# Kernel optimization log

Measured on AMD Instinct MI355X. Metric: run time of the kernel, lower is better.

## Reference

```python
import jax, jax.numpy as jnp
import numpy as np


def setup_inputs() -> dict:
    B, S, DK, DV, H = 2, 2048, 1024, 1024, 16
    ks = jax.random.split(jax.random.key(0), 7)
    keys = jax.random.normal(ks[0], (B, S, DK), jnp.float32)
    queries = jax.random.normal(ks[1], (B, S, DK), jnp.float32)
    values = jax.random.normal(ks[2], (B, S, DV), jnp.float32)
    # per-head projection weights, stored as [H, in, out] (torch Linear uses W.T; math-equivalent)
    WQ = jax.random.normal(ks[3], (H, DK, DK // H), jnp.float32) / np.sqrt(DK).astype(np.float32)
    WK = jax.random.normal(ks[4], (H, DK, DK // H), jnp.float32) / np.sqrt(DK).astype(np.float32)
    WV = jax.random.normal(ks[5], (H, DV, DV // H), jnp.float32) / np.sqrt(DV).astype(np.float32)
    WO = jax.random.normal(ks[6], (DV, DV), jnp.float32) / np.sqrt(DV).astype(np.float32)
    return {"keys": keys, "queries": queries, "values": values,
            "WQ": WQ, "WK": WK, "WV": WV, "WO": WO, "masking": 1}


def reference(keys, queries, values, WQ, WK, WV, WO, masking):
    B, Sq, _ = queries.shape
    Sk = keys.shape[1]
    # batched per-head projections (original loops over heads in Python)
    Q = jnp.einsum('bqd,hde->bhqe', queries, WQ)   # [B,H,Sq,dh]
    K = jnp.einsum('bkd,hde->bhke', keys, WK)      # [B,H,Sk,dh]
    V = jnp.einsum('bkd,hde->bhke', values, WV)    # [B,H,Sk,dvh]
    q_idx = jnp.arange(Sq)[:, None]
    k_idx = jnp.arange(Sk)[None, :]
    causal = k_idx <= q_idx
    # NOTE: original never applies the slope m; bias = (i - j) for i<=j else 0, same for all heads
    bias = jnp.where(causal, (k_idx - q_idx).astype(jnp.float32), 0.0)
    scale = np.float32(1.0 / np.sqrt(Sk))  # original divides by sqrt(keys.shape[1])
    y = (jnp.einsum('bhqe,bhke->bhqk', Q, K) + bias) * scale
    if masking:
        y = jnp.where(causal, y, -jnp.inf)
    # original: F.softmax(y, 1) on [B,Sq,Sk] -> softmax over the QUERY axis
    z = jax.nn.softmax(y, axis=2)
    out = jnp.einsum('bhqk,bhke->bhqe', z, V)      # [B,H,Sq,dvh]
    out = out.transpose(0, 2, 1, 3).reshape(B, Sq, -1)  # concat heads on last dim
    return out @ WO
```

## Files before the change

### kernel.cpp

```cpp
#include <hip/hip_runtime.h>
#include <math.h>

#define SEQ    2048
#define DMODEL 1024
#define NH     16
#define DH     64
#define NB     2
#define BHN    (NB*NH)

static constexpr float SCALE = 0.02209708691207961f;

typedef __attribute__((ext_vector_type(8))) short short8;
typedef __attribute__((ext_vector_type(4))) short short4v;
typedef __attribute__((ext_vector_type(4))) float f32x4;

__device__ __forceinline__ short f2bf(float f) {
    union { float f; unsigned u; } v; v.f = f;
    unsigned r = (v.u + 0x7FFFu + ((v.u >> 16) & 1u)) >> 16;
    return (short)r;
}

__device__ __forceinline__ unsigned pack_bf2(float a, float b) {
    union { float f; unsigned u; } ua, ub; ua.f = a; ub.f = b;
    return __builtin_amdgcn_perm(ub.u + 0x8000u, ua.u + 0x8000u, 0x07060302u);
}

__device__ __forceinline__ float bf2f(short s) {
    union { unsigned u; float f; } v; v.u = ((unsigned)(unsigned short)s) << 16;
    return v.f;
}

__device__ __forceinline__ void load16_lds(const short* g, short* l) {
    __builtin_amdgcn_global_load_lds(
        (const __attribute__((address_space(1))) unsigned int*)g,
        (__attribute__((address_space(3))) unsigned int*)l,
        16, 0, 0);
}

__device__ __forceinline__ void stage_rows(const short* g, short* s, int t, int ldg, int nIter) {
    int wave = t >> 6, lane = t & 63;
    #pragma unroll
    for (int i = 0; i < 4; ++i) {
        if (i >= nIter) break;
        int E   = i * 2048 + wave * 512 + lane * 8;
        int row = E >> 6;
        int blk = (lane & 7) ^ (row & 7);
        load16_lds(g + (size_t)row * ldg + blk * 8, s + i * 2048 + wave * 512);
    }
}

__device__ __forceinline__ short8 frag_sw(const short* s, int rowbase, int ks, int lane) {
    int m   = rowbase + (lane & 15);
    int q   = lane >> 4;
    int blk = (ks * 4 + q) ^ (m & 7);
    return *(const short8*)(s + m * 64 + blk * 8);
}

__global__ __launch_bounds__(256) void convert_x(
    const float* __restrict__ q, const float* __restrict__ k, const float* __restrict__ v,
    short* __restrict__ Xq, short* __restrict__ Xk, short* __restrict__ Xv)
{
    const int z = blockIdx.z;
    const float* src = (z == 0) ? q : (z == 1) ? k : v;
    short* dst = (z == 0) ? Xq : (z == 1) ? Xk : Xv;
    size_t idx = ((size_t)blockIdx.x * 256 + threadIdx.x) * 8;
    float4 a = *(const float4*)(src + idx);
    float4 b = *(const float4*)(src + idx + 4);
    short8 o;
    o[0] = f2bf(a.x); o[1] = f2bf(a.y); o[2] = f2bf(a.z); o[3] = f2bf(a.w);
    o[4] = f2bf(b.x); o[5] = f2bf(b.y); o[6] = f2bf(b.z); o[7] = f2bf(b.w);
    *(short8*)(dst + idx) = o;
}

__global__ __launch_bounds__(256) void convert_w(
    const float* __restrict__ WQ, const float* __restrict__ WK,
    const float* __restrict__ WV, const float* __restrict__ WO,
    short* __restrict__ WQt, short* __restrict__ WKt,
    short* __restrict__ WVt, short* __restrict__ WOt)
{
    const int z = blockIdx.z;
    const int k0 = blockIdx.x * 64;
    const int ny = blockIdx.y;
    const float* W = (z == 0) ? WQ : (z == 1) ? WK : (z == 2) ? WV : WO;
    short* Wt = (z == 0) ? WQt : (z == 1) ? WKt : (z == 2) ? WVt : WOt;

    __shared__ float Ts[64][68];
    const int t = threadIdx.x;
    const int tr = t >> 4, tc4 = (t & 15) * 4;

    #pragma unroll
    for (int i = 0; i < 4; ++i) {
        int row = tr + i * 16;
        float4 v;
        if (z < 3) v = *(const float4*)(W + (size_t)ny * DMODEL * DH + (size_t)(k0 + row) * DH + tc4);
        else       v = *(const float4*)(W + (size_t)(k0 + row) * DMODEL + ny * 64 + tc4);
        Ts[tc4 + 0][row] = v.x; Ts[tc4 + 1][row] = v.y;
        Ts[tc4 + 2][row] = v.z; Ts[tc4 + 3][row] = v.w;
    }
    __syncthreads();
    #pragma unroll
    for (int i = 0; i < 4; ++i) {
        int nl = tr + i * 16;
        short4v o;
        o[0] = f2bf(Ts[nl][tc4 + 0]); o[1] = f2bf(Ts[nl][tc4 + 1]);
        o[2] = f2bf(Ts[nl][tc4 + 2]); o[3] = f2bf(Ts[nl][tc4 + 3]);
        *(short4v*)(Wt + (size_t)(ny * 64 + nl) * DMODEL + k0 + tc4) = o;
    }
}

__global__ __launch_bounds__(256) void gemm_nt(
    const short* __restrict__ A0, const short* __restrict__ A1, const short* __restrict__ A2,
    const short* __restrict__ B0, const short* __restrict__ B1, const short* __restrict__ B2,
    short* __restrict__ Y0, short* __restrict__ Y1, short* __restrict__ Y2,
    float* __restrict__ outF, float* __restrict__ outF2, int phase)
{
    const int z = blockIdx.z;
    const short* X  = (phase == 1) ? A0 : (z == 0) ? A0 : (z == 1) ? A1 : A2;
    const short* Wt = (phase == 1) ? B0 : (z == 0) ? B0 : (z == 1) ? B1 : B2;
    short* Y        = (z == 0) ? Y0 : (z == 1) ? Y1 : Y2;
    const bool vOrient = (phase == 0) && (z == 2);

    const int lin = blockIdx.y * 8 + blockIdx.x;
    const int n0 = (lin >> 5) * 128;
    const int m0 = (lin & 31) * 128;

    __shared__ short As[128 * 64];
    __shared__ short Bs[128 * 64];

    const int t = threadIdx.x;
    const int wave = t >> 6, lane = t & 63;
    const int wrow = (wave >> 1) * 64, wcol = (wave & 1) * 64;
    const int quad = lane >> 4, l15 = lane & 15;

    f32x4 acc[4][4];
    #pragma unroll
    for (int i = 0; i < 4; ++i)
        #pragma unroll
        for (int j = 0; j < 4; ++j)
            acc[i][j] = (f32x4)0.f;

    const int kBeg = (phase == 1) ? (z * 512) : 0;
    const int kEnd = (phase == 1) ? (z * 512 + 512) : DMODEL;
    for (int k0 = kBeg; k0 < kEnd; k0 += 64) {
        __syncthreads();
        stage_rows(X  + (size_t)m0 * DMODEL + k0, As, t, DMODEL, 4);
        stage_rows(Wt + (size_t)n0 * DMODEL + k0, Bs, t, DMODEL, 4);
        __syncthreads();
        if (!vOrient) {
            #pragma unroll
            for (int ks = 0; ks < 2; ++ks) {
                short8 xf[4], wf[4];
                #pragma unroll
                for (int i = 0; i < 4; ++i) xf[i] = frag_sw(As, wrow + i * 16, ks, lane);
                #pragma unroll
                for (int i = 0; i < 4; ++i) wf[i] = frag_sw(Bs, wcol + i * 16, ks, lane);
                #pragma unroll
                for (int a = 0; a < 4; ++a)
                    #pragma unroll
                    for (int b = 0; b < 4; ++b)
                        acc[a][b] = __builtin_amdgcn_mfma_f32_16x16x32_bf16(
                            wf[a], xf[b], acc[a][b], 0, 0, 0);
            }
        } else {
            #pragma unroll
            for (int ks = 0; ks < 2; ++ks) {
                short8 xf[4], wf[4];
                #pragma unroll
                for (int i = 0; i < 4; ++i) xf[i] = frag_sw(As, wrow + i * 16, ks, lane);
                #pragma unroll
                for (int i = 0; i < 4; ++i) wf[i] = frag_sw(Bs, wcol + i * 16, ks, lane);
                #pragma unroll
                for (int a = 0; a < 4; ++a)
                    #pragma unroll
                    for (int b = 0; b < 4; ++b)
                        acc[a][b] = __builtin_amdgcn_mfma_f32_16x16x32_bf16(
                            xf[a], wf[b], acc[a][b], 0, 0, 0);
            }
        }
    }

    if (vOrient) {
        #pragma unroll
        for (int a = 0; a < 4; ++a) {
            #pragma unroll
            for (int b = 0; b < 4; ++b) {
                int m = m0 + wrow + a * 16 + quad * 4;
                int n = n0 + wcol + b * 16 + l15;
                int bb = m >> 11, s = m & 2047, h = n >> 6, e = n & 63;
                short4v o;
                #pragma unroll
                for (int i = 0; i < 4; ++i) o[i] = f2bf(acc[a][b][i]);
                *(short4v*)(Y + ((size_t)((bb * NH + h) * DH + e)) * SEQ + s) = o;
            }
        }
    } else if (phase == 1) {
        float* dst = (z == 0) ? outF : outF2;
        #pragma unroll
        for (int a = 0; a < 4; ++a) {
            #pragma unroll
            for (int b = 0; b < 4; ++b) {
                int n = n0 + wcol + a * 16 + quad * 4;
                int m = m0 + wrow + b * 16 + l15;
                float4 o = make_float4(acc[a][b][0], acc[a][b][1], acc[a][b][2], acc[a][b][3]);
                *(float4*)(dst + (size_t)m * DMODEL + n) = o;
            }
        }
    } else {
        #pragma unroll
        for (int a = 0; a < 4; ++a) {
            #pragma unroll
            for (int b = 0; b < 4; ++b) {
                int n = n0 + wcol + a * 16 + quad * 4;
                int m = m0 + wrow + b * 16 + l15;
                int bb = m >> 11, s = m & 2047, h = n >> 6, e = n & 63;
                short4v o;
                #pragma unroll
                for (int i = 0; i < 4; ++i) o[i] = f2bf(acc[a][b][i]);
                *(short4v*)(Y + ((size_t)((bb * NH + h) * SEQ + s)) * DH + e) = o;
            }
        }
    }
}

__global__ __launch_bounds__(256) void reduce_add(
    float* __restrict__ dst, const float* __restrict__ src)
{
    size_t i = ((size_t)blockIdx.x * 256 + threadIdx.x) * 8;
    float4 a0 = *(float4*)(dst + i);
    float4 a1 = *(float4*)(dst + i + 4);
    float4 b0 = *(const float4*)(src + i);
    float4 b1 = *(const float4*)(src + i + 4);
    a0.x += b0.x; a0.y += b0.y; a0.z += b0.z; a0.w += b0.w;
    a1.x += b1.x; a1.y += b1.y; a1.z += b1.z; a1.w += b1.w;
    *(float4*)(dst + i) = a0;
    *(float4*)(dst + i + 4) = a1;
}

__global__ __launch_bounds__(256) void stats_mfma(
    const short* __restrict__ Qg, const short* __restrict__ Kg,
    float* __restrict__ rDg, const int* __restrict__ mask_p)
{
    const int gblk = blockIdx.x;
    const int masking = mask_p[0];

    __shared__ short Ks[64 * 64];
    __shared__ short Qs[2][128 * 64];

    const int t = threadIdx.x;
    const int wave = t >> 6, lane = t & 63;
    const int quad = lane >> 4, l15 = lane & 15;

    for (int item = 0; item < 2; ++item) {
        const int w  = item ? (1023 - gblk) : gblk;
        const int kt = w >> 5, bh = w & 31;
        const int k0 = kt * 64;

        const int qb0 = masking ? (kt >> 1) : 0;
        const int q0s = qb0 * 128;
        if (item) __syncthreads();
        stage_rows(Kg + ((size_t)bh * SEQ + k0) * DH, Ks, t, DH, 2);
        stage_rows(Qg + ((size_t)bh * SEQ + q0s) * DH, Qs[0], t, DH, 4);
        __syncthreads();

        short8 Kf[2];
        Kf[0] = frag_sw(Ks, wave * 16, 0, lane);
        Kf[1] = frag_sw(Ks, wave * 16, 1, lane);

        int   kgi[4];
        float biasK[4];
        #pragma unroll
        for (int i = 0; i < 4; ++i) {
            kgi[i] = k0 + wave * 16 + quad * 4 + i;
            biasK[i] = SCALE * (float)kgi[i];
        }
        float qS[8];
        #pragma unroll
        for (int nt = 0; nt < 8; ++nt)
            qS[nt] = SCALE * (float)(q0s + nt * 16 + l15);

        float dsum[4] = {0.f, 0.f, 0.f, 0.f};
        const int nIter = masking ? (16 - qb0) : 16;
        for (int it = 0; it < nIter; ++it) {
            const int cur = it & 1;
            if (it > 0) __syncthreads();
            if (it + 1 < nIter)
                stage_rows(Qg + ((size_t)bh * SEQ + q0s + (it + 1) * 128) * DH, Qs[1 - cur], t, DH, 4);

            f32x4 acc[8];
            #pragma unroll
            for (int nt = 0; nt < 8; ++nt) acc[nt] = (f32x4)0.f;
            __builtin_amdgcn_s_setprio(1);
            #pragma unroll
            for (int ks = 0; ks < 2; ++ks)
                #pragma unroll
                for (int nt = 0; nt < 8; ++nt)
                    acc[nt] = __builtin_amdgcn_mfma_f32_16x16x32_bf16(
                        Kf[ks], frag_sw(Qs[cur], nt * 16, ks, lane), acc[nt], 0, 0, 0);
            __builtin_amdgcn_s_setprio(0);

            const bool exact = masking && (it == 0);
            #pragma unroll
            for (int nt = 0; nt < 8; ++nt) {
                #pragma unroll
                for (int i = 0; i < 4; ++i) {
                    float diff = biasK[i] - qS[nt];
                    float v = masking ? fmaf(acc[nt][i], SCALE, diff)
                                      : fmaf(acc[nt][i], SCALE, fminf(diff, 0.f));
                    float e = __expf(v);
                    if (exact)
                        e = (kgi[i] <= (q0s + nt * 16 + l15)) ? e : 0.f;
                    dsum[i] += e;
                }
            }
            #pragma unroll
            for (int nt = 0; nt < 8; ++nt) qS[nt] += 128.f * SCALE;
        }

        #pragma unroll
        for (int i = 0; i < 4; ++i) {
            float d = dsum[i];
            #pragma unroll
            for (int mm = 1; mm < 16; mm <<= 1) d += __shfl_xor(d, mm);
            dsum[i] = d;
        }
        if (l15 == 0) {
            const int kc = k0 + wave * 16 + quad * 4;
            float4 o = make_float4(1.f / dsum[0], 1.f / dsum[1], 1.f / dsum[2], 1.f / dsum[3]);
            *(float4*)(rDg + (size_t)bh * SEQ + kc) = o;
        }
    }
}

__global__ __launch_bounds__(256) void scale_vt(
    short* __restrict__ Vt, const float* __restrict__ rDg)
{
    size_t base = ((size_t)blockIdx.x * 256 + threadIdx.x) * 8;
    int s = (int)(base & (SEQ - 1));
    int bh = (int)(base >> 17);
    short8 v = *(short8*)(Vt + base);
    const float* rp = rDg + (size_t)bh * SEQ + s;
    float4 r0 = *(const float4*)rp;
    float4 r1 = *(const float4*)(rp + 4);
    float rr[8] = {r0.x, r0.y, r0.z, r0.w, r1.x, r1.y, r1.z, r1.w};
    union { unsigned u[4]; short8 s8; } o;
    #pragma unroll
    for (int j = 0; j < 4; ++j)
        o.u[j] = pack_bf2(bf2f(v[2 * j]) * rr[2 * j], bf2f(v[2 * j + 1]) * rr[2 * j + 1]);
    *(short8*)(Vt + base) = o.s8;
}

template<int MODE>
__device__ __forceinline__ void attn_tile(
    const short* Kbuf, const short* Vbuf, short* Pw,
    const short8 Qf[2], const float bias[4][4], f32x4 oacc[4],
    int lane, int quad, int l15, int qloc)
{
    f32x4 sacc[4];
    #pragma unroll
    for (int mt = 0; mt < 4; ++mt) sacc[mt] = (f32x4)0.f;
    __builtin_amdgcn_s_setprio(1);
    #pragma unroll
    for (int ks = 0; ks < 2; ++ks) {
        #pragma unroll
        for (int mt = 0; mt < 4; ++mt)
            sacc[mt] = __builtin_amdgcn_mfma_f32_16x16x32_bf16(
                frag_sw(Kbuf, mt * 16, ks, lane), Qf[ks], sacc[mt], 0, 0, 0);
    }
    __builtin_amdgcn_s_setprio(0);
    __asm__ volatile("" ::: "memory");
    #pragma unroll
    for (int mt = 0; mt < 4; ++mt) {
        float p[4];
        #pragma unroll
        for (int i = 0; i < 4; ++i) {
            float bi = bias[mt][i];
            float v = (MODE == 2) ? fmaf(sacc[mt][i], SCALE, fminf(bi, 0.f))
                                  : fmaf(sacc[mt][i], SCALE, bi);
            float e = __expf(v);
            if (MODE == 1)
                e = ((mt * 16 + quad * 4 + i) <= qloc) ? e : 0.f;
            p[i] = e;
        }
        int blk = (2 * mt + (quad >> 1)) ^ (l15 & 7);
        *(uint2*)(Pw + l15 * 64 + blk * 8 + (quad & 1) * 4) =
            make_uint2(pack_bf2(p[0], p[1]), pack_bf2(p[2], p[3]));
    }
    __asm__ volatile("" ::: "memory");
    __builtin_amdgcn_s_setprio(1);
    #pragma unroll
    for (int ks = 0; ks < 2; ++ks) {
        short8 pf = *(const short8*)(Pw + l15 * 64 + (((ks * 4 + quad) ^ (l15 & 7)) * 8));
        #pragma unroll
        for (int mt = 0; mt < 4; ++mt)
            oacc[mt] = __builtin_amdgcn_mfma_f32_16x16x32_bf16(
                frag_sw(Vbuf, mt * 16, ks, lane), pf, oacc[mt], 0, 0, 0);
    }
    __builtin_amdgcn_s_setprio(0);
}

__global__ __launch_bounds__(256) void attn_mfma(
    const short* __restrict__ Qg, const short* __restrict__ Kg, const short* __restrict__ Vt,
    short* __restrict__ attnb, const int* __restrict__ mask_p)
{
    const int gblk = blockIdx.x;
    const int masking = mask_p[0];

    __shared__ short Qs[64 * 64];
    __shared__ short Ks[2][64 * 64];
    __shared__ short Vts[2][64 * 64];

    const int t = threadIdx.x;
    const int wave = t >> 6, lane = t & 63;
    const int quad = lane >> 4, l15 = lane & 15;
    short* Pw = Qs + wave * 1024;
    const int qloc = wave * 16 + l15;

    for (int item = 0; item < 2; ++item) {
        const int w  = item ? (1023 - gblk) : gblk;
        const int qt = w >> 5, bh = w & 31;
        const int b = bh >> 4, h = bh & (NH - 1);
        const int q0 = qt * 64;

        if (item) __syncthreads();
        stage_rows(Qg + ((size_t)bh * SEQ + q0) * DH, Qs, t, DH, 2);
        stage_rows(Kg + (size_t)bh * SEQ * DH, Ks[0], t, DH, 2);
        stage_rows(Vt + (size_t)bh * DH * SEQ, Vts[0], t, SEQ, 2);
        __syncthreads();

        short8 Qf[2];
        Qf[0] = frag_sw(Qs, wave * 16, 0, lane);
        Qf[1] = frag_sw(Qs, wave * 16, 1, lane);

        float bias[4][4];
        #pragma unroll
        for (int mt = 0; mt < 4; ++mt)
            #pragma unroll
            for (int i = 0; i < 4; ++i)
                bias[mt][i] = SCALE * (float)((mt * 16 + quad * 4 + i)
                                            - (q0 + qloc));

        f32x4 oacc[4];
        #pragma unroll
        for (int mt = 0; mt < 4; ++mt) oacc[mt] = (f32x4)0.f;

        const int nIter = masking ? (qt + 1) : (SEQ / 64);
        for (int it = 0; it < nIter; ++it) {
            const int cur = it & 1;
            if (it > 0) __syncthreads();
            if (it + 1 < nIter) {
                const int k0n = (it + 1) * 64;
                stage_rows(Kg + ((size_t)bh * SEQ + k0n) * DH, Ks[1 - cur], t, DH, 2);
                stage_rows(Vt + (size_t)bh * DH * SEQ + k0n, Vts[1 - cur], t, SEQ, 2);
            }
            if (!masking)       attn_tile<2>(Ks[cur], Vts[cur], Pw, Qf, bias, oacc, lane, quad, l15, qloc);
            else if (it == qt)  attn_tile<1>(Ks[cur], Vts[cur], Pw, Qf, bias, oacc, lane, quad, l15, qloc);
            else                attn_tile<0>(Ks[cur], Vts[cur], Pw, Qf, bias, oacc, lane, quad, l15, qloc);
            #pragma unroll
            for (int mt = 0; mt < 4; ++mt)
                #pragma unroll
                for (int i = 0; i < 4; ++i)
                    bias[mt][i] += 64.f * SCALE;
        }

        #pragma unroll
        for (int mt = 0; mt < 4; ++mt) {
            int e = mt * 16 + quad * 4;
            int q = q0 + wave * 16 + l15;
            short4v o;
            #pragma unroll
            for (int i = 0; i < 4; ++i) o[i] = f2bf(oacc[mt][i]);
            *(short4v*)(attnb + ((size_t)(b * SEQ + q)) * DMODEL + h * DH + e) = o;
        }
    }
}

extern "C" void kernel_launch(void* const* d_in, const int* in_sizes, int n_in,
                              void* d_out, int out_size, void* d_ws, size_t ws_size,
                              hipStream_t stream) {
    const float* keys    = (const float*)d_in[0];
    const float* queries = (const float*)d_in[1];
    const float* values  = (const float*)d_in[2];
    const float* WQ      = (const float*)d_in[3];
    const float* WK      = (const float*)d_in[4];
    const float* WV      = (const float*)d_in[5];
    const float* WO      = (const float*)d_in[6];
    const int*   mask_p  = (const int*)d_in[7];
    float* out = (float*)d_out;

    const size_t nX = (size_t)NB * SEQ * DMODEL;
    const size_t nW = (size_t)DMODEL * DMODEL;
    const size_t nQ = (size_t)BHN * SEQ * DH;

    short* ws = (short*)d_ws;
    short* Xq    = ws;
    short* Xk    = Xq + nX;
    short* Xv    = Xk + nX;
    short* WQt   = Xv + nX;
    short* WKt   = WQt + nW;
    short* WVt   = WKt + nW;
    short* WOt   = WVt + nW;
    short* Qg    = WOt + nW;
    short* Kg    = Qg + nQ;
    short* Vtg   = Kg + nQ;
    short* attnb = Vtg + nQ;
    float* rDg   = (float*)(attnb + nX);
    float* outP1 = (float*)ws;

    convert_x<<<dim3(2048, 1, 3), dim3(256), 0, stream>>>(queries, keys, values, Xq, Xk, Xv);
    convert_w<<<dim3(16, 16, 4), dim3(256), 0, stream>>>(WQ, WK, WV, WO, WQt, WKt, WVt, WOt);
    gemm_nt<<<dim3(8, 32, 3), dim3(256), 0, stream>>>(
        Xq, Xk, Xv, WQt, WKt, WVt, Qg, Kg, Vtg, nullptr, nullptr, 0);
    stats_mfma<<<dim3(512), dim3(256), 0, stream>>>(Qg, Kg, rDg, mask_p);
    scale_vt<<<dim3(2048), dim3(256), 0, stream>>>(Vtg, rDg);
    attn_mfma<<<dim3(512), dim3(256), 0, stream>>>(Qg, Kg, Vtg, attnb, mask_p);
    gemm_nt<<<dim3(8, 32, 2), dim3(256), 0, stream>>>(
        attnb, nullptr, nullptr, WOt, nullptr, nullptr, nullptr, nullptr, nullptr, out, outP1, 1);
    reduce_add<<<dim3(2048), dim3(256), 0, stream>>>(out, outP1);
}
```

Measured before the change: 258.0 us.

## Fold column-normalizer into attention P and double-buffer output projection GEMM

Drops the separate scale_vt kernel. The per-key reciprocal denominators are instead applied to the exponentiated scores inside attn_tile, which saves a full read-modify-write pass over V and one launch. The output projection gets its own kernel, gemm_out, with double-buffered shared-memory staging so loads overlap the MFMA work; the phase branches leave gemm_nt. In exchange the attention inner loop does an extra global float4 load per tile, and gemm_out doubles its LDS use, which may lower occupancy.

```diff
diff --git a/kernel.cpp b/kernel.cpp
--- a/kernel.cpp
+++ b/kernel.cpp
@@ -111,14 +111,13 @@
 __global__ __launch_bounds__(256) void gemm_nt(
     const short* __restrict__ A0, const short* __restrict__ A1, const short* __restrict__ A2,
     const short* __restrict__ B0, const short* __restrict__ B1, const short* __restrict__ B2,
-    short* __restrict__ Y0, short* __restrict__ Y1, short* __restrict__ Y2,
-    float* __restrict__ outF, float* __restrict__ outF2, int phase)
+    short* __restrict__ Y0, short* __restrict__ Y1, short* __restrict__ Y2)
 {
     const int z = blockIdx.z;
-    const short* X  = (phase == 1) ? A0 : (z == 0) ? A0 : (z == 1) ? A1 : A2;
-    const short* Wt = (phase == 1) ? B0 : (z == 0) ? B0 : (z == 1) ? B1 : B2;
+    const short* X  = (z == 0) ? A0 : (z == 1) ? A1 : A2;
+    const short* Wt = (z == 0) ? B0 : (z == 1) ? B1 : B2;
     short* Y        = (z == 0) ? Y0 : (z == 1) ? Y1 : Y2;
-    const bool vOrient = (phase == 0) && (z == 2);
+    const bool vOrient = (z == 2);
 
     const int lin = blockIdx.y * 8 + blockIdx.x;
     const int n0 = (lin >> 5) * 128;
@@ -139,9 +138,7 @@
         for (int j = 0; j < 4; ++j)
             acc[i][j] = (f32x4)0.f;
 
-    const int kBeg = (phase == 1) ? (z * 512) : 0;
-    const int kEnd = (phase == 1) ? (z * 512 + 512) : DMODEL;
-    for (int k0 = kBeg; k0 < kEnd; k0 += 64) {
+    for (int k0 = 0; k0 < DMODEL; k0 += 64) {
         __syncthreads();
         stage_rows(X  + (size_t)m0 * DMODEL + k0, As, t, DMODEL, 4);
         stage_rows(Wt + (size_t)n0 * DMODEL + k0, Bs, t, DMODEL, 4);
@@ -193,18 +190,6 @@
                 *(short4v*)(Y + ((size_t)((bb * NH + h) * DH + e)) * SEQ + s) = o;
             }
         }
-    } else if (phase == 1) {
-        float* dst = (z == 0) ? outF : outF2;
-        #pragma unroll
-        for (int a = 0; a < 4; ++a) {
-            #pragma unroll
-            for (int b = 0; b < 4; ++b) {
-                int n = n0 + wcol + a * 16 + quad * 4;
-                int m = m0 + wrow + b * 16 + l15;
-                float4 o = make_float4(acc[a][b][0], acc[a][b][1], acc[a][b][2], acc[a][b][3]);
-                *(float4*)(dst + (size_t)m * DMODEL + n) = o;
-            }
-        }
     } else {
         #pragma unroll
         for (int a = 0; a < 4; ++a) {
@@ -218,6 +203,73 @@
                 for (int i = 0; i < 4; ++i) o[i] = f2bf(acc[a][b][i]);
                 *(short4v*)(Y + ((size_t)((bb * NH + h) * SEQ + s)) * DH + e) = o;
             }
+        }
+    }
+}
+
+__global__ __launch_bounds__(256) void gemm_out(
+    const short* __restrict__ X, const short* __restrict__ Wt,
+    float* __restrict__ o0, float* __restrict__ o1)
+{
+    const int z = blockIdx.z;
+    const int lin = blockIdx.y * 8 + blockIdx.x;
+    const int n0 = (lin >> 5) * 128;
+    const int m0 = (lin & 31) * 128;
+
+    __shared__ short As[2][128 * 64];
+    __shared__ short Bs[2][128 * 64];
+
+    const int t = threadIdx.x;
+    const int wave = t >> 6, lane = t & 63;
+    const int wrow = (wave >> 1) * 64, wcol = (wave & 1) * 64;
+    const int quad = lane >> 4, l15 = lane & 15;
+
+    f32x4 acc[4][4];
+    #pragma unroll
+    for (int i = 0; i < 4; ++i)
+        #pragma unroll
+        for (int j = 0; j < 4; ++j)
+            acc[i][j] = (f32x4)0.f;
+
+    const int kBeg = z * 512;
+    stage_rows(X  + (size_t)m0 * DMODEL + kBeg, As[0], t, DMODEL, 4);
+    stage_rows(Wt + (size_t)n0 * DMODEL + kBeg, Bs[0], t, DMODEL, 4);
+    __syncthreads();
+
+    int cur = 0;
+    for (int it = 0; it < 8; ++it) {
+        if (it + 1 < 8) {
+            const int k0 = kBeg + (it + 1) * 64;
+            stage_rows(X  + (size_t)m0 * DMODEL + k0, As[cur ^ 1], t, DMODEL, 4);
+            stage_rows(Wt + (size_t)n0 * DMODEL + k0, Bs[cur ^ 1], t, DMODEL, 4);
+        }
+        #pragma unroll
+        for (int ks = 0; ks < 2; ++ks) {
+            short8 xf[4], wf[4];
+            #pragma unroll
+            for (int i = 0; i < 4; ++i) xf[i] = frag_sw(As[cur], wrow + i * 16, ks, lane);
+            #pragma unroll
+            for (int i = 0; i < 4; ++i) wf[i] = frag_sw(Bs[cur], wcol + i * 16, ks, lane);
+            #pragma unroll
+            for (int a = 0; a < 4; ++a)
+                #pragma unroll
+                for (int b = 0; b < 4; ++b)
+                    acc[a][b] = __builtin_amdgcn_mfma_f32_16x16x32_bf16(
+                        wf[a], xf[b], acc[a][b], 0, 0, 0);
+        }
+        __syncthreads();
+        cur ^= 1;
+    }
+
+    float* dst = z ? o1 : o0;
+    #pragma unroll
+    for (int a = 0; a < 4; ++a) {
+        #pragma unroll
+        for (int b = 0; b < 4; ++b) {
+            int n = n0 + wcol + a * 16 + quad * 4;
+            int m = m0 + wrow + b * 16 + l15;
+            float4 o = make_float4(acc[a][b][0], acc[a][b][1], acc[a][b][2], acc[a][b][3]);
+            *(float4*)(dst + (size_t)m * DMODEL + n) = o;
         }
     }
 }
@@ -331,28 +383,11 @@
     }
 }
 
-__global__ __launch_bounds__(256) void scale_vt(
-    short* __restrict__ Vt, const float* __restrict__ rDg)
-{
-    size_t base = ((size_t)blockIdx.x * 256 + threadIdx.x) * 8;
-    int s = (int)(base & (SEQ - 1));
-    int bh = (int)(base >> 17);
-    short8 v = *(short8*)(Vt + base);
-    const float* rp = rDg + (size_t)bh * SEQ + s;
-    float4 r0 = *(const float4*)rp;
-    float4 r1 = *(const float4*)(rp + 4);
-    float rr[8] = {r0.x, r0.y, r0.z, r0.w, r1.x, r1.y, r1.z, r1.w};
-    union { unsigned u[4]; short8 s8; } o;
-    #pragma unroll
-    for (int j = 0; j < 4; ++j)
-        o.u[j] = pack_bf2(bf2f(v[2 * j]) * rr[2 * j], bf2f(v[2 * j + 1]) * rr[2 * j + 1]);
-    *(short8*)(Vt + base) = o.s8;
-}
-
 template<int MODE>
 __device__ __forceinline__ void attn_tile(
     const short* Kbuf, const short* Vbuf, short* Pw,
     const short8 Qf[2], const float bias[4][4], f32x4 oacc[4],
+    const float* __restrict__ rDk,
     int lane, int quad, int l15, int qloc)
 {
     f32x4 sacc[4];
@@ -370,6 +405,8 @@
     __asm__ volatile("" ::: "memory");
     #pragma unroll
     for (int mt = 0; mt < 4; ++mt) {
+        float4 rv4 = *(const float4*)(rDk + mt * 16 + quad * 4);
+        float rv[4] = {rv4.x, rv4.y, rv4.z, rv4.w};
         float p[4];
         #pragma unroll
         for (int i = 0; i < 4; ++i) {
@@ -379,7 +416,7 @@
             float e = __expf(v);
             if (MODE == 1)
                 e = ((mt * 16 + quad * 4 + i) <= qloc) ? e : 0.f;
-            p[i] = e;
+            p[i] = e * rv[i];
         }
         int blk = (2 * mt + (quad >> 1)) ^ (l15 & 7);
         *(uint2*)(Pw + l15 * 64 + blk * 8 + (quad & 1) * 4) =
@@ -400,7 +437,7 @@
 
 __global__ __launch_bounds__(256) void attn_mfma(
     const short* __restrict__ Qg, const short* __restrict__ Kg, const short* __restrict__ Vt,
-    short* __restrict__ attnb, const int* __restrict__ mask_p)
+    const float* __restrict__ rDg, short* __restrict__ attnb, const int* __restrict__ mask_p)
 {
     const int gblk = blockIdx.x;
     const int masking = mask_p[0];
@@ -420,6 +457,7 @@
         const int qt = w >> 5, bh = w & 31;
         const int b = bh >> 4, h = bh & (NH - 1);
         const int q0 = qt * 64;
+        const float* rDb = rDg + (size_t)bh * SEQ;
 
         if (item) __syncthreads();
         stage_rows(Qg + ((size_t)bh * SEQ + q0) * DH, Qs, t, DH, 2);
@@ -452,9 +490,10 @@
                 stage_rows(Kg + ((size_t)bh * SEQ + k0n) * DH, Ks[1 - cur], t, DH, 2);
                 stage_rows(Vt + (size_t)bh * DH * SEQ + k0n, Vts[1 - cur], t, SEQ, 2);
             }
-            if (!masking)       attn_tile<2>(Ks[cur], Vts[cur], Pw, Qf, bias, oacc, lane, quad, l15, qloc);
-            else if (it == qt)  attn_tile<1>(Ks[cur], Vts[cur], Pw, Qf, bias, oacc, lane, quad, l15, qloc);
-            else                attn_tile<0>(Ks[cur], Vts[cur], Pw, Qf, bias, oacc, lane, quad, l15, qloc);
+            const float* rDk = rDb + it * 64;
+            if (!masking)       attn_tile<2>(Ks[cur], Vts[cur], Pw, Qf, bias, oacc, rDk, lane, quad, l15, qloc);
+            else if (it == qt)  attn_tile<1>(Ks[cur], Vts[cur], Pw, Qf, bias, oacc, rDk, lane, quad, l15, qloc);
+            else                attn_tile<0>(Ks[cur], Vts[cur], Pw, Qf, bias, oacc, rDk, lane, quad, l15, qloc);
             #pragma unroll
             for (int mt = 0; mt < 4; ++mt)
                 #pragma unroll
@@ -509,11 +548,9 @@
     convert_x<<<dim3(2048, 1, 3), dim3(256), 0, stream>>>(queries, keys, values, Xq, Xk, Xv);
     convert_w<<<dim3(16, 16, 4), dim3(256), 0, stream>>>(WQ, WK, WV, WO, WQt, WKt, WVt, WOt);
     gemm_nt<<<dim3(8, 32, 3), dim3(256), 0, stream>>>(
-        Xq, Xk, Xv, WQt, WKt, WVt, Qg, Kg, Vtg, nullptr, nullptr, 0);
+        Xq, Xk, Xv, WQt, WKt, WVt, Qg, Kg, Vtg);
     stats_mfma<<<dim3(512), dim3(256), 0, stream>>>(Qg, Kg, rDg, mask_p);
-    scale_vt<<<dim3(2048), dim3(256), 0, stream>>>(Vtg, rDg);
-    attn_mfma<<<dim3(512), dim3(256), 0, stream>>>(Qg, Kg, Vtg, attnb, mask_p);
-    gemm_nt<<<dim3(8, 32, 2), dim3(256), 0, stream>>>(
-        attnb, nullptr, nullptr, WOt, nullptr, nullptr, nullptr, nullptr, nullptr, out, outP1, 1);
+    attn_mfma<<<dim3(512), dim3(256), 0, stream>>>(Qg, Kg, Vtg, rDg, attnb, mask_p);
+    gemm_out<<<dim3(8, 32, 2), dim3(256), 0, stream>>>(attnb, WOt, out, outP1);
     reduce_add<<<dim3(2048), dim3(256), 0, stream>>>(out, outP1);
 }
```

Measured after the change: 257.8 us. Within noise of the previous version (-0.1%).
